# Kernel optimization log

Measured on AMD Instinct MI355X. Metric: run time of the kernel, lower is better.

Reference implementation:

```python
import jax, jax.numpy as jnp
import numpy as np
from jax import lax

EPS = 1e-5

def conv2d(x, w, groups=1, pad=0):
    return lax.conv_general_dilated(
        x, w, window_strides=(1, 1), padding=[(pad, pad), (pad, pad)],
        dimension_numbers=('NCHW', 'OIHW', 'NCHW'), feature_group_count=groups)

def setup_inputs() -> dict:
    key = jax.random.key(0)
    ks = jax.random.split(key, 10)
    B, C, H, W = 8, 64, 128, 128
    s = 0.05
    f32 = jnp.float32
    return {
        'x': jax.random.normal(ks[0], (B, C, H, W), f32),
        # key_embed: Conv2d(64,64,3,groups=8,bias=False) -> weight [64, 64/8, 3, 3]
        'w_key': jax.random.normal(ks[1], (64, 8, 3, 3), f32) * s,
        # embed[0]: Conv2d(128,32,1,groups=2,bias=False) -> [32, 128/2, 1, 1]
        'w_e1': jax.random.normal(ks[2], (32, 64, 1, 1), f32) * s,
        # embed[2]: Conv2d(32,72,1,groups=2,bias=True) -> [72, 32/2, 1, 1]
        'w_e2': jax.random.normal(ks[3], (72, 16, 1, 1), f32) * s,
        'b_e2': jax.random.normal(ks[4], (72,), f32) * s,
        # GroupNorm(num_groups=8, num_channels=72) affine params
        'gn_w': jnp.ones((72,), f32),
        'gn_b': jnp.zeros((72,), f32),
        # conv1x1: Conv2d(64,64,1,groups=2,bias=False) -> [64, 32, 1, 1]
        'w_c1': jax.random.normal(ks[5], (64, 32, 1, 1), f32) * s,
        # conv_du: Conv2d(64,4,1,bias=False), Conv2d(4,64,1,bias=False)
        'w_du1': jax.random.normal(ks[6], (4, 64, 1, 1), f32) * s,
        'w_du2': jax.random.normal(ks[7], (64, 4, 1, 1), f32) * s,
    }

def reference(x, w_key, w_e1, w_e2, b_e2, gn_w, gn_b, w_c1, w_du1, w_du2):
    B, C, H, W = x.shape  # C == 64
    KK = 9                # kernel_size^2
    # key embedding: grouped 3x3 conv + ReLU
    k = jax.nn.relu(conv2d(x, w_key, groups=8, pad=1))
    # interleave x and k along channels: view of [B,64,2,H,W] -> [B,128,H,W]
    qk = jnp.stack([x, k], axis=2).reshape(B, 2 * C, H, W)
    # dynamic kernel generation (embed)
    w = jax.nn.relu(conv2d(qk, w_e1, groups=2))
    w = conv2d(w, w_e2, groups=2) + b_e2[None, :, None, None]  # [B,72,H,W]
    # GroupNorm(8, 72): normalize over (channels-in-group, H, W)
    wg = w.reshape(B, 8, 9, H, W)
    m = wg.mean(axis=(2, 3, 4), keepdims=True)
    v = wg.var(axis=(2, 3, 4), keepdims=True)
    w = ((wg - m) * lax.rsqrt(v + EPS)).reshape(B, 72, H, W)
    w = w * gn_w[None, :, None, None] + gn_b[None, :, None, None]
    # per-pixel kernels: [B*2, 4, 9, H, W]
    w = w.reshape(B * 2, 4, KK, H, W)
    # value path
    xv = conv2d(x, w_c1, groups=2).reshape(B * 2, 32, H, W)
    # unfold 3x3 patches with zero padding 1 -> [B*2, 32, 9, H, W]
    xp = jnp.pad(xv, ((0, 0), (0, 0), (1, 1), (1, 1)))
    patches = jnp.stack(
        [xp[:, :, i:i + H, j:j + W] for i in range(3) for j in range(3)], axis=2)
    # share_planes=8: 8 channels share each kernel -> [B*2, 4, 8, 9, H, W]
    patches = patches.reshape(B * 2, 4, 8, KK, H, W)
    out = jnp.einsum('bgckhw,bgkhw->bgchw', patches, w)  # local conv
    out = out.reshape(B, C, H, W)
    # channel attention
    y = out.mean(axis=(2, 3))                 # [B, 64]
    y = jax.nn.relu(y @ w_du1[:, :, 0, 0].T)  # [B, 4]
    y = jax.nn.sigmoid(y @ w_du2[:, :, 0, 0].T)  # [B, 64]
    return out * y[:, :, None, None]
```

## Files before the change

kernel.cpp:

```cpp
#include <hip/hip_runtime.h>
#include <math.h>

#define Hd 128
#define Wd 128
#define HW 16384

__device__ __forceinline__ float wred(float v) {
  #pragma unroll
  for (int o = 32; o > 0; o >>= 1) v += __shfl_down(v, o, 64);
  return v;
}

__global__ __launch_bounds__(256) void k_fused(const float* __restrict__ x,
                                               const float* __restrict__ wkey,
                                               const float* __restrict__ we1,
                                               const float* __restrict__ we2,
                                               const float* __restrict__ be2,
                                               const float* __restrict__ wc1,
                                               float* __restrict__ xv,
                                               float* __restrict__ w1out,
                                               float* __restrict__ spart) {
  __shared__ float xt[8][18][24];
  __shared__ float sred2[4][8];
  const int tid = threadIdx.x;
  const int tx = tid & 15, ty = tid >> 4;
  const int b = blockIdx.y, s = blockIdx.z;
  const int h0 = (blockIdx.x >> 3) * 16, w0 = (blockIdx.x & 7) * 16;
  const int p = ((h0 + ty) << 7) + (w0 + tx);
  float xc[32], kc[32];
  #pragma unroll
  for (int g = 0; g < 4; ++g) {
    for (int i = tid; i < 8 * 324; i += 256) {
      int ch = i / 324, r = i - ch * 324;
      int yy = r / 18, xx = r - yy * 18;
      int gh = h0 + yy - 1, gw = w0 + xx - 1;
      float v = 0.f;
      if (gh >= 0 && gh < Hd && gw >= 0 && gw < Wd)
        v = x[((long)(b * 64 + 32 * s + 8 * g + ch) << 14) + (gh << 7) + gw];
      xt[ch][yy][xx] = v;
    }
    __syncthreads();
    float kacc[8] = {0.f, 0.f, 0.f, 0.f, 0.f, 0.f, 0.f, 0.f};
    const float* wg = wkey + (4 * s + g) * 576;
    #pragma unroll
    for (int ich = 0; ich < 8; ++ich) {
      float nb[9];
      #pragma unroll
      for (int rr = 0; rr < 3; ++rr)
        #pragma unroll
        for (int cc = 0; cc < 3; ++cc)
          nb[rr * 3 + cc] = xt[ich][ty + rr][tx + cc];
      xc[8 * g + ich] = nb[4];
      #pragma unroll
      for (int oc = 0; oc < 8; ++oc) {
        const float* wr = wg + oc * 72 + ich * 9;
        #pragma unroll
        for (int k9 = 0; k9 < 9; ++k9) kacc[oc] += wr[k9] * nb[k9];
      }
    }
    #pragma unroll
    for (int oc = 0; oc < 8; ++oc) kc[8 * g + oc] = fmaxf(kacc[oc], 0.f);
    __syncthreads();
  }
  #pragma unroll 4
  for (int o = 0; o < 32; ++o) {
    const float* wr = wc1 + (32 * s + o) * 32;
    float a = 0.f;
    #pragma unroll
    for (int j = 0; j < 32; ++j) a += wr[j] * xc[j];
    xv[((long)(b * 64 + 32 * s + o) << 14) + p] = a;
  }
  float w1a[16];
  #pragma unroll
  for (int o = 0; o < 16; ++o) {
    const float* wr = we1 + (16 * s + o) * 64;
    float a = 0.f;
    #pragma unroll
    for (int j = 0; j < 32; ++j) a += wr[2 * j] * xc[j] + wr[2 * j + 1] * kc[j];
    w1a[o] = fmaxf(a, 0.f);
    w1out[((long)(b * 32 + 16 * s + o) << 14) + p] = w1a[o];
  }
  #pragma unroll
  for (int gl = 0; gl < 4; ++gl) {
    float lgs = 0.f, lgq = 0.f;
    #pragma unroll
    for (int kk = 0; kk < 9; ++kk) {
      const int oc2 = 36 * s + gl * 9 + kk;
      const float* wr = we2 + oc2 * 16;
      float a = be2[oc2];
      #pragma unroll
      for (int ic = 0; ic < 16; ++ic) a += wr[ic] * w1a[ic];
      lgs += a;
      lgq += a * a;
    }
    float r1 = wred(lgs), r2 = wred(lgq);
    if ((tid & 63) == 0) {
      sred2[tid >> 6][2 * gl] = r1;
      sred2[tid >> 6][2 * gl + 1] = r2;
    }
  }
  __syncthreads();
  if (tid < 8) {
    float a = sred2[0][tid] + sred2[1][tid] + sred2[2][tid] + sred2[3][tid];
    spart[blockIdx.x * 128 + b * 16 + s * 8 + tid] = a;
  }
}

__global__ __launch_bounds__(256) void k_local(const float* __restrict__ xv,
                                               const float* __restrict__ w1in,
                                               const float* __restrict__ we2,
                                               const float* __restrict__ be2,
                                               const float* __restrict__ spart,
                                               const float* __restrict__ gnw,
                                               const float* __restrict__ gnb,
                                               float* __restrict__ out,
                                               float* __restrict__ part) {
  __shared__ float xt[8][34][24];
  __shared__ float sminv[2];
  const int tid = threadIdx.x;
  const int tx = tid & 15, ty = tid >> 4;
  const int z = blockIdx.z;
  const int b2 = z >> 2, g = z & 3;
  const int t = b2 & 1, b = b2 >> 1;
  const int gg = 4 * t + g;
  const int h0 = blockIdx.y * 32, w0 = blockIdx.x * 16;
  for (int i = tid; i < 8 * 612; i += 256) {
    int ch = i / 612, r = i - ch * 612;
    int yy = r / 18, xx = r - yy * 18;
    int gh = h0 + yy - 1, gw = w0 + xx - 1;
    float v = 0.f;
    if (gh >= 0 && gh < Hd && gw >= 0 && gw < Wd)
      v = xv[((long)(b * 64 + t * 32 + g * 8 + ch) << 14) + (gh << 7) + gw];
    xt[ch][yy][xx] = v;
  }
  if (tid < 64) {
    const float* sp = spart + tid * 128 + (b * 8 + gg) * 2;
    float sv = sp[0], qv = sp[1];
    #pragma unroll
    for (int o = 32; o > 0; o >>= 1) {
      sv += __shfl_down(sv, o, 64);
      qv += __shfl_down(qv, o, 64);
    }
    if (tid == 0) {
      const float N = 9.f * (float)HW;
      float mm = sv / N;
      float var = qv / N - mm * mm;
      sminv[0] = mm;
      sminv[1] = rsqrtf(var + 1e-5f);
    }
  }
  __syncthreads();
  const float m = sminv[0];
  const float inv = sminv[1];
  const int p0 = ((h0 + 2 * ty) << 7) + (w0 + tx);
  const int p1 = p0 + 128;
  float wn0[9], wn1[9];
  {
    float v[16];
    #pragma unroll
    for (int o = 0; o < 16; ++o)
      v[o] = w1in[((long)(b * 32 + t * 16 + o) << 14) + p0];
    #pragma unroll
    for (int kk = 0; kk < 9; ++kk) {
      const int ch72 = 36 * t + 9 * g + kk;
      const float* wr = we2 + ch72 * 16;
      float a = be2[ch72];
      #pragma unroll
      for (int ic = 0; ic < 16; ++ic) a += wr[ic] * v[ic];
      const float sc = inv * gnw[ch72];
      wn0[kk] = a * sc + (gnb[ch72] - m * sc);
    }
    #pragma unroll
    for (int o = 0; o < 16; ++o)
      v[o] = w1in[((long)(b * 32 + t * 16 + o) << 14) + p1];
    #pragma unroll
    for (int kk = 0; kk < 9; ++kk) {
      const int ch72 = 36 * t + 9 * g + kk;
      const float* wr = we2 + ch72 * 16;
      float a = be2[ch72];
      #pragma unroll
      for (int ic = 0; ic < 16; ++ic) a += wr[ic] * v[ic];
      const float sc = inv * gnw[ch72];
      wn1[kk] = a * sc + (gnb[ch72] - m * sc);
    }
  }
  const int prow = (blockIdx.y * 8 + blockIdx.x) * 4 + (tid >> 6);
  #pragma unroll
  for (int cc = 0; cc < 8; ++cc) {
    float nb[12];
    #pragma unroll
    for (int rr = 0; rr < 4; ++rr)
      #pragma unroll
      for (int ccol = 0; ccol < 3; ++ccol)
        nb[rr * 3 + ccol] = xt[cc][2 * ty + rr][tx + ccol];
    float o0 = 0.f, o1 = 0.f;
    #pragma unroll
    for (int dy = 0; dy < 3; ++dy)
      #pragma unroll
      for (int dx = 0; dx < 3; ++dx) {
        o0 += wn0[dy * 3 + dx] * nb[dy * 3 + dx];
        o1 += wn1[dy * 3 + dx] * nb[(dy + 1) * 3 + dx];
      }
    const int ch512 = b2 * 32 + g * 8 + cc;
    out[((long)ch512 << 14) + p0] = o0;
    out[((long)ch512 << 14) + p1] = o1;
    float os = wred(o0 + o1);
    if ((tid & 63) == 0) part[prow * 512 + ch512] = os;
  }
}

__global__ void k_ca(const float* __restrict__ part, const float* __restrict__ du1,
                     const float* __restrict__ du2, float* __restrict__ ys) {
  __shared__ float sy[8][64];
  __shared__ float sy4[8][4];
  const int tid = threadIdx.x;
  const int b = tid >> 6, c = tid & 63;
  float acc = 0.f;
  #pragma unroll 8
  for (int r = 0; r < 128; ++r) acc += part[r * 512 + tid];
  sy[b][c] = acc * (1.f / (float)HW);
  __syncthreads();
  if (tid < 32) {
    int bb = tid >> 2, j = tid & 3;
    float a = 0.f;
    for (int c2 = 0; c2 < 64; ++c2) a += sy[bb][c2] * du1[j * 64 + c2];
    sy4[bb][j] = fmaxf(a, 0.f);
  }
  __syncthreads();
  float z = 0.f;
  #pragma unroll
  for (int j = 0; j < 4; ++j) z += sy4[b][j] * du2[c * 4 + j];
  ys[tid] = 1.f / (1.f + expf(-z));
}

__global__ __launch_bounds__(256) void k_scale(float* __restrict__ out,
                                               const float* __restrict__ ys) {
  const long i4 = (long)blockIdx.x * 256 + threadIdx.x;
  const long e = i4 * 4;
  const int bc = (int)(e >> 14);
  const float s = ys[bc];
  float4* o = (float4*)out;
  float4 v = o[i4];
  v.x *= s; v.y *= s; v.z *= s; v.w *= s;
  o[i4] = v;
}

extern "C" void kernel_launch(void* const* d_in, const int* in_sizes, int n_in,
                              void* d_out, int out_size, void* d_ws, size_t ws_size,
                              hipStream_t stream) {
  const float* x    = (const float*)d_in[0];
  const float* wkey = (const float*)d_in[1];
  const float* we1  = (const float*)d_in[2];
  const float* we2  = (const float*)d_in[3];
  const float* be2  = (const float*)d_in[4];
  const float* gnw  = (const float*)d_in[5];
  const float* gnb  = (const float*)d_in[6];
  const float* wc1  = (const float*)d_in[7];
  const float* du1  = (const float*)d_in[8];
  const float* du2  = (const float*)d_in[9];
  float* out = (float*)d_out;
  float* ws = (float*)d_ws;

  float* xv   = ws;
  float* w1a  = ws + 8388608;
  float* part = ws + 12582912;
  float* spart = part + 65536;
  float* ys   = spart + 8192;

  k_fused<<<dim3(64, 8, 2), 256, 0, stream>>>(x, wkey, we1, we2, be2, wc1, xv, w1a, spart);
  k_local<<<dim3(8, 4, 64), 256, 0, stream>>>(xv, w1a, we2, be2, spart, gnw, gnb, out, part);
  k_ca<<<1, 512, 0, stream>>>(part, du1, du2, ys);
  k_scale<<<8192, 256, 0, stream>>>(out, ys);
}
```

Baseline: 226.1 us.

## Double-buffer halo tile loads in fused kernel and parallelize channel-attention across batches

The fused kernel now prefetches the next channel group's 18x18 halo tile into registers while computing the grouped 3x3 conv on the current group. It then commits that tile to a second shared-memory buffer, which removes one barrier per group and hides global load latency. The channel-attention kernel is split into one block per batch, with a two-level row reduction, instead of a single 512-thread block summing 128 rows serially. The cost is 11 more live registers per thread in a kernel that already holds many arrays, plus double the shared-memory tile.

```diff
diff --git a/kernel.cpp b/kernel.cpp
--- a/kernel.cpp
+++ b/kernel.cpp
@@ -20,26 +20,53 @@
                                                float* __restrict__ xv,
                                                float* __restrict__ w1out,
                                                float* __restrict__ spart) {
-  __shared__ float xt[8][18][24];
+  __shared__ float xt[2][8][18][24];
   __shared__ float sred2[4][8];
   const int tid = threadIdx.x;
   const int tx = tid & 15, ty = tid >> 4;
   const int b = blockIdx.y, s = blockIdx.z;
   const int h0 = (blockIdx.x >> 3) * 16, w0 = (blockIdx.x & 7) * 16;
   const int p = ((h0 + ty) << 7) + (w0 + tx);
+
+  auto issue = [&](int g, float* pre) {
+    #pragma unroll
+    for (int k = 0; k < 11; ++k) {
+      const int i = tid + k * 256;
+      if (i < 2592) {
+        int ch = i / 324, r = i - ch * 324;
+        int yy = r / 18, xx = r - yy * 18;
+        int gh = h0 + yy - 1, gw = w0 + xx - 1;
+        float v = 0.f;
+        if (gh >= 0 && gh < Hd && gw >= 0 && gw < Wd)
+          v = x[((long)(b * 64 + 32 * s + 8 * g + ch) << 14) + (gh << 7) + gw];
+        pre[k] = v;
+      }
+    }
+  };
+  auto commit = [&](int buf, const float* pre) {
+    #pragma unroll
+    for (int k = 0; k < 11; ++k) {
+      const int i = tid + k * 256;
+      if (i < 2592) {
+        int ch = i / 324, r = i - ch * 324;
+        int yy = r / 18, xx = r - yy * 18;
+        xt[buf][ch][yy][xx] = pre[k];
+      }
+    }
+  };
+
   float xc[32], kc[32];
+  {
+    float pre0[11];
+    issue(0, pre0);
+    commit(0, pre0);
+  }
+  __syncthreads();
+  float preN[11];
   #pragma unroll
   for (int g = 0; g < 4; ++g) {
-    for (int i = tid; i < 8 * 324; i += 256) {
-      int ch = i / 324, r = i - ch * 324;
-      int yy = r / 18, xx = r - yy * 18;
-      int gh = h0 + yy - 1, gw = w0 + xx - 1;
-      float v = 0.f;
-      if (gh >= 0 && gh < Hd && gw >= 0 && gw < Wd)
-        v = x[((long)(b * 64 + 32 * s + 8 * g + ch) << 14) + (gh << 7) + gw];
-      xt[ch][yy][xx] = v;
-    }
-    __syncthreads();
+    if (g < 3) issue(g + 1, preN);
+    const int cur = g & 1;
     float kacc[8] = {0.f, 0.f, 0.f, 0.f, 0.f, 0.f, 0.f, 0.f};
     const float* wg = wkey + (4 * s + g) * 576;
     #pragma unroll
@@ -49,7 +76,7 @@
       for (int rr = 0; rr < 3; ++rr)
         #pragma unroll
         for (int cc = 0; cc < 3; ++cc)
-          nb[rr * 3 + cc] = xt[ich][ty + rr][tx + cc];
+          nb[rr * 3 + cc] = xt[cur][ich][ty + rr][tx + cc];
       xc[8 * g + ich] = nb[4];
       #pragma unroll
       for (int oc = 0; oc < 8; ++oc) {
@@ -60,6 +87,7 @@
     }
     #pragma unroll
     for (int oc = 0; oc < 8; ++oc) kc[8 * g + oc] = fmaxf(kacc[oc], 0.f);
+    if (g < 3) commit((g + 1) & 1, preN);
     __syncthreads();
   }
   #pragma unroll 4
@@ -211,26 +239,36 @@
 
 __global__ void k_ca(const float* __restrict__ part, const float* __restrict__ du1,
                      const float* __restrict__ du2, float* __restrict__ ys) {
-  __shared__ float sy[8][64];
-  __shared__ float sy4[8][4];
+  __shared__ float red[8][64];
+  __shared__ float sy[64];
+  __shared__ float sy4[4];
+  const int b = blockIdx.x;
   const int tid = threadIdx.x;
-  const int b = tid >> 6, c = tid & 63;
+  const int c = tid & 63, rc = tid >> 6;
   float acc = 0.f;
-  #pragma unroll 8
-  for (int r = 0; r < 128; ++r) acc += part[r * 512 + tid];
-  sy[b][c] = acc * (1.f / (float)HW);
-  __syncthreads();
-  if (tid < 32) {
-    int bb = tid >> 2, j = tid & 3;
+  #pragma unroll
+  for (int r = rc; r < 128; r += 8) acc += part[r * 512 + b * 64 + c];
+  red[rc][c] = acc;
+  __syncthreads();
+  if (tid < 64) {
     float a = 0.f;
-    for (int c2 = 0; c2 < 64; ++c2) a += sy[bb][c2] * du1[j * 64 + c2];
-    sy4[bb][j] = fmaxf(a, 0.f);
-  }
-  __syncthreads();
-  float z = 0.f;
-  #pragma unroll
-  for (int j = 0; j < 4; ++j) z += sy4[b][j] * du2[c * 4 + j];
-  ys[tid] = 1.f / (1.f + expf(-z));
+    #pragma unroll
+    for (int k = 0; k < 8; ++k) a += red[k][tid];
+    sy[tid] = a * (1.f / (float)HW);
+  }
+  __syncthreads();
+  if (tid < 4) {
+    float a = 0.f;
+    for (int c2 = 0; c2 < 64; ++c2) a += sy[c2] * du1[tid * 64 + c2];
+    sy4[tid] = fmaxf(a, 0.f);
+  }
+  __syncthreads();
+  if (tid < 64) {
+    float z = 0.f;
+    #pragma unroll
+    for (int j = 0; j < 4; ++j) z += sy4[j] * du2[tid * 4 + j];
+    ys[b * 64 + tid] = 1.f / (1.f + expf(-z));
+  }
 }
 
 __global__ __launch_bounds__(256) void k_scale(float* __restrict__ out,
@@ -269,6 +307,6 @@
 
   k_fused<<<dim3(64, 8, 2), 256, 0, stream>>>(x, wkey, we1, we2, be2, wc1, xv, w1a, spart);
   k_local<<<dim3(8, 4, 64), 256, 0, stream>>>(xv, w1a, we2, be2, spart, gnw, gnb, out, part);
-  k_ca<<<1, 512, 0, stream>>>(part, du1, du2, ys);
+  k_ca<<<8, 512, 0, stream>>>(part, du1, du2, ys);
   k_scale<<<8192, 256, 0, stream>>>(out, ys);
 }
```

New measurement: 425.1 us. +88.0%, slower.
